# Optimization experiments

Measured on AMD Instinct MI355X. Metric: run time of the kernel, lower is better.

## Reference

```python
import jax, jax.numpy as jnp
import numpy as np

B, T, EMB, HS = 512, 256, 364, 64

def setup_inputs() -> dict:
    key = jax.random.key(0)
    ks = jax.random.split(key, 7)
    s = EMB ** -0.5  # keep weight scale sane
    return {
        "x": jax.random.normal(ks[0], (B, T, EMB), jnp.float32),
        "Wk": jax.random.normal(ks[1], (EMB, HS), jnp.float32) * s,
        "bk": jax.random.normal(ks[2], (HS,), jnp.float32) * 0.01,
        "Wq": jax.random.normal(ks[3], (EMB, HS), jnp.float32) * s,
        "bq": jax.random.normal(ks[4], (HS,), jnp.float32) * 0.01,
        "Wv": jax.random.normal(ks[5], (EMB, HS), jnp.float32) * s,
        "bv": jax.random.normal(ks[6], (HS,), jnp.float32) * 0.01,
    }

def reference(x, Wk, bk, Wq, bq, Wv, bv):
    # Faithful to the original: wei = k @ q^T (note swapped q/k vs textbook),
    # scaled by head_size**-0.5, causal mask, softmax, (dropout = identity in eval), then @ v.
    k = x @ Wk + bk          # [B, T, HS]
    q = x @ Wq + bq          # [B, T, HS]
    v = x @ Wv + bv          # [B, T, HS]
    scale = k.shape[-1] ** -0.5
    wei = jnp.einsum('btd,bsd->bts', k, q) * scale  # [B, T, T]
    causal = jnp.tril(jnp.ones((T, T), dtype=bool))
    wei = jnp.where(causal, wei, -jnp.inf)
    wei = jax.nn.softmax(wei, axis=-1)
    out = jnp.einsum('bts,bsd->btd', wei, v)        # [B, T, HS]
    return out
```

## Files before the change

### kernel.cpp

```cpp
#include <hip/hip_runtime.h>
#include <math.h>

#define BB   512
#define TT   256
#define EMBD 364
#define HS   64
#define KPAD 384
#define NC   192

typedef __attribute__((ext_vector_type(8))) short short8_t;
typedef __attribute__((ext_vector_type(4))) float f32x4;

__device__ __forceinline__ ushort f2bf(float v) {
    union { float f; unsigned u; } c; c.f = v;
    unsigned b = c.u;
    return (ushort)((b + 0x7FFF + ((b >> 16) & 1)) >> 16);
}
__device__ __forceinline__ ushort f2bfc(float v) {
    union { float f; unsigned u; } c; c.f = v;
    return (ushort)((c.u + 0x8000u) >> 16);
}

#define GLOAD_LDS16(GP, LP)                                                       \
    __builtin_amdgcn_global_load_lds(                                             \
        (const __attribute__((address_space(1))) void*)(const void*)(GP),         \
        (__attribute__((address_space(3))) void*)(void*)(LP), 16, 0, 0)

#define WTR_BYTES ((size_t)144 * 512 * 2)
#define KQ_ELEMS  ((size_t)BB * TT * HS)
#define K_OFF_B   (WTR_BYTES)
#define Q_OFF_B   (K_OFF_B + KQ_ELEMS * 2)
#define VT_OFF_B  (Q_OFF_B + KQ_ELEMS * 2)

__global__ void prep_wtr(const float* __restrict__ Wk, const float* __restrict__ Wq,
                         const float* __restrict__ Wv, ushort* __restrict__ WTr)
{
    const int bid = blockIdx.x;
    const int jj  = bid / 12;
    const int t   = bid % 12;
    const int l   = threadIdx.x;
    const int c   = jj * 16 + (l & 15);
    const float* Wp = (c < 64) ? Wk : (c < 128 ? Wq : Wv);
    const float s   = (c < 64) ? 0.125f : 1.0f;
    const int col   = c & 63;
    #pragma unroll
    for (int i = 0; i < 8; ++i) {
        int k = t * 32 + (l >> 4) * 8 + i;
        float v = (k < EMBD) ? Wp[(size_t)k * HS + col] * s : 0.f;
        WTr[((size_t)bid * 64 + l) * 8 + i] = f2bf(v);
    }
}

__global__ __launch_bounds__(256, 3) void proj_gemm(
    const float* __restrict__ x, const ushort* __restrict__ WTr,
    const float* __restrict__ bk_, const float* __restrict__ bq_,
    const float* __restrict__ bv_,
    ushort* __restrict__ Kg, ushort* __restrict__ Qg, ushort* __restrict__ Vt)
{
    const int blk = blockIdx.x;
    const int tid = threadIdx.x;
    const int l   = tid & 63;
    const int w   = tid >> 6;
    const int l15 = l & 15;
    const int lg  = l >> 4;

    __shared__ float xf[32 * KPAD];

    const float* xb = x + (size_t)blk * 32 * EMBD;

    #pragma unroll
    for (int gi = 0; gi < 12; ++gi) {
        const int g     = w * 12 + gi;
        const unsigned flatP = (unsigned)(g * 64 + l);
        const unsigned row   = flatP / 96u;
        const unsigned p     = flatP % 96u;
        const unsigned q     = p ^ (row & 7u);
        const unsigned colq  = (q < 91u) ? q : 0u;
        const float* gp = xb + (size_t)row * EMBD + colq * 4u;
        GLOAD_LDS16(gp, (char*)xf + (size_t)g * 1024);
    }

    float bias3[3];
    #pragma unroll
    for (int j = 0; j < 3; ++j) {
        int c = w * 48 + j * 16 + l15;
        bias3[j] = (c < 64) ? bk_[c] * 0.125f : (c < 128 ? bq_[c - 64] : bv_[c - 128]);
    }

    f32x4 acc[2][3];
    #pragma unroll
    for (int mi = 0; mi < 2; ++mi)
        #pragma unroll
        for (int j = 0; j < 3; ++j) acc[mi][j] = (f32x4){0.f, 0.f, 0.f, 0.f};

    __syncthreads();

    #pragma unroll
    for (int ks = 0; ks < 12; ++ks) {
        short8_t Bf[3];
        #pragma unroll
        for (int j = 0; j < 3; ++j)
            Bf[j] = *(const short8_t*)&WTr[(((size_t)(w * 3 + j) * 12 + ks) * 64 + l) * 8];
        #pragma unroll
        for (int mi = 0; mi < 2; ++mi) {
            const unsigned row = mi * 16 + l15;
            const unsigned q0  = ks * 8 + lg * 2;
            const unsigned p0  = q0 ^ (row & 7u);
            const unsigned p1  = (q0 + 1u) ^ (row & 7u);
            f32x4 A0 = *(const f32x4*)&xf[row * KPAD + p0 * 4u];
            f32x4 A1 = *(const f32x4*)&xf[row * KPAD + p1 * 4u];
            union { short8_t s8; ushort us[8]; } pk;
            pk.us[0] = f2bfc(A0[0]); pk.us[1] = f2bfc(A0[1]);
            pk.us[2] = f2bfc(A0[2]); pk.us[3] = f2bfc(A0[3]);
            pk.us[4] = f2bfc(A1[0]); pk.us[5] = f2bfc(A1[1]);
            pk.us[6] = f2bfc(A1[2]); pk.us[7] = f2bfc(A1[3]);
            #pragma unroll
            for (int j = 0; j < 3; ++j)
                acc[mi][j] = __builtin_amdgcn_mfma_f32_16x16x32_bf16(pk.s8, Bf[j], acc[mi][j], 0, 0, 0);
        }
    }

    const int b   = blk >> 3;
    const int tl0 = (blk & 7) * 32;
    #pragma unroll
    for (int j = 0; j < 3; ++j) {
        const int c = w * 48 + j * 16 + l15;
        #pragma unroll
        for (int mi = 0; mi < 2; ++mi) {
            if (c < 64) {
                #pragma unroll
                for (int r = 0; r < 4; ++r) {
                    const size_t trow = (size_t)blk * 32 + mi * 16 + lg * 4 + r;
                    Kg[trow * HS + c] = f2bf(acc[mi][j][r] + bias3[j]);
                }
            } else if (c < 128) {
                #pragma unroll
                for (int r = 0; r < 4; ++r) {
                    const size_t trow = (size_t)blk * 32 + mi * 16 + lg * 4 + r;
                    Qg[trow * HS + (c - 64)] = f2bf(acc[mi][j][r] + bias3[j]);
                }
            } else {
                ushort4 pk;
                pk.x = f2bf(acc[mi][j][0] + bias3[j]);
                pk.y = f2bf(acc[mi][j][1] + bias3[j]);
                pk.z = f2bf(acc[mi][j][2] + bias3[j]);
                pk.w = f2bf(acc[mi][j][3] + bias3[j]);
                *(ushort4*)&Vt[((size_t)b * HS + (c - 128)) * TT + tl0 + mi * 16 + lg * 4] = pk;
            }
        }
    }
}

__global__ __launch_bounds__(512, 4) void attn_fused(
    const ushort* __restrict__ Kg, const ushort* __restrict__ Qg,
    const ushort* __restrict__ Vt, float* __restrict__ out)
{
    const int b   = blockIdx.x;
    const int tid = threadIdx.x;
    const int l   = tid & 63;
    const int w   = tid >> 6;
    const int l15 = l & 15;
    const int lg  = l >> 4;

    __shared__ ushort pb[8][16 * 40];
    ushort* pbw = pb[w];

    const ushort* Kb = Kg + (size_t)b * TT * HS;
    const ushort* Qb = Qg + (size_t)b * TT * HS;
    const ushort* Vb = Vt + (size_t)b * HS * TT;

    #pragma unroll
    for (int half = 0; half < 2; ++half) {
        const int rt = half ? (15 - w) : w;
        const int t0 = rt * 16;

        short8_t afr[2];
        afr[0] = *(const short8_t*)&Kb[(t0 + l15) * HS + lg * 8];
        afr[1] = *(const short8_t*)&Kb[(t0 + l15) * HS + 32 + lg * 8];

        float mr[4], lr[4];
        f32x4 o[4];
        #pragma unroll
        for (int r = 0; r < 4; ++r) { mr[r] = -INFINITY; lr[r] = 0.f; }
        #pragma unroll
        for (int nt = 0; nt < 4; ++nt) o[nt] = (f32x4){0.f, 0.f, 0.f, 0.f};

        const int jd = t0 >> 5;
        for (int j = 0; j <= jd; ++j) {
            const int sb = j * 32;
            f32x4 sacc[2];
            sacc[0] = (f32x4){0.f, 0.f, 0.f, 0.f};
            sacc[1] = (f32x4){0.f, 0.f, 0.f, 0.f};
            #pragma unroll
            for (int kk = 0; kk < 2; ++kk) {
                #pragma unroll
                for (int ct = 0; ct < 2; ++ct) {
                    short8_t bfr = *(const short8_t*)&Qb[(sb + ct * 16 + l15) * HS + kk * 32 + lg * 8];
                    sacc[ct] = __builtin_amdgcn_mfma_f32_16x16x32_bf16(afr[kk], bfr, sacc[ct], 0, 0, 0);
                }
            }
            #pragma unroll
            for (int ct = 0; ct < 2; ++ct) {
                int s = sb + ct * 16 + l15;
                #pragma unroll
                for (int r = 0; r < 4; ++r) {
                    int t = t0 + lg * 4 + r;
                    if (s > t) sacc[ct][r] = -INFINITY;
                }
            }
            float p0[4], p1[4], fsc[4];
            #pragma unroll
            for (int r = 0; r < 4; ++r) {
                float mx = fmaxf(sacc[0][r], sacc[1][r]);
                mx = fmaxf(mx, __shfl_xor(mx, 1));
                mx = fmaxf(mx, __shfl_xor(mx, 2));
                mx = fmaxf(mx, __shfl_xor(mx, 4));
                mx = fmaxf(mx, __shfl_xor(mx, 8));
                float nm = fmaxf(mr[r], mx);
                fsc[r] = __expf(mr[r] - nm);
                mr[r] = nm;
                p0[r] = __expf(sacc[0][r] - nm);
                p1[r] = __expf(sacc[1][r] - nm);
                float ps = p0[r] + p1[r];
                ps += __shfl_xor(ps, 1);
                ps += __shfl_xor(ps, 2);
                ps += __shfl_xor(ps, 4);
                ps += __shfl_xor(ps, 8);
                lr[r] = lr[r] * fsc[r] + ps;
            }
            #pragma unroll
            for (int nt = 0; nt < 4; ++nt)
                #pragma unroll
                for (int r = 0; r < 4; ++r) o[nt][r] *= fsc[r];
            #pragma unroll
            for (int r = 0; r < 4; ++r) {
                pbw[(lg * 4 + r) * 40 + l15]      = f2bf(p0[r]);
                pbw[(lg * 4 + r) * 40 + 16 + l15] = f2bf(p1[r]);
            }
            short8_t pa = *(const short8_t*)&pbw[l15 * 40 + lg * 8];
            #pragma unroll
            for (int nt = 0; nt < 4; ++nt) {
                short8_t bfr = *(const short8_t*)&Vb[(nt * 16 + l15) * TT + sb + lg * 8];
                o[nt] = __builtin_amdgcn_mfma_f32_16x16x32_bf16(pa, bfr, o[nt], 0, 0, 0);
            }
        }
        #pragma unroll
        for (int r = 0; r < 4; ++r) {
            float inv = 1.0f / lr[r];
            int t = t0 + lg * 4 + r;
            float* op = out + ((size_t)b * TT + t) * HS;
            #pragma unroll
            for (int nt = 0; nt < 4; ++nt)
                op[nt * 16 + l15] = o[nt][r] * inv;
        }
    }
}

extern "C" void kernel_launch(void* const* d_in, const int* in_sizes, int n_in,
                              void* d_out, int out_size, void* d_ws, size_t ws_size,
                              hipStream_t stream) {
    const float* x  = (const float*)d_in[0];
    const float* Wk = (const float*)d_in[1];
    const float* bk = (const float*)d_in[2];
    const float* Wq = (const float*)d_in[3];
    const float* bq = (const float*)d_in[4];
    const float* Wv = (const float*)d_in[5];
    const float* bv = (const float*)d_in[6];
    float* out = (float*)d_out;

    ushort* WTr = (ushort*)d_ws;
    ushort* Kg  = (ushort*)((char*)d_ws + K_OFF_B);
    ushort* Qg  = (ushort*)((char*)d_ws + Q_OFF_B);
    ushort* Vt  = (ushort*)((char*)d_ws + VT_OFF_B);

    prep_wtr<<<dim3(144), dim3(64), 0, stream>>>(Wk, Wq, Wv, WTr);
    proj_gemm<<<dim3(4096), dim3(256), 0, stream>>>(x, WTr, bk, bq, bv, Kg, Qg, Vt);
    attn_fused<<<dim3(BB), dim3(512), 0, stream>>>(Kg, Qg, Vt, out);
}
```

Before: 112.2 us.

## Split projection into separate bf16 cast pass and bf16-input GEMM

Adds an xcast kernel that converts x to padded bf16 in workspace, then a proj_bf GEMM that loads bf16 rows into LDS and feeds MFMA directly, removing the per-tile fp32-to-bf16 conversion and halving LDS footprint so more blocks fit per CU. It costs an extra full pass over x (read fp32 plus write and re-read bf16, about 100MB of extra traffic) and an extra launch. The old fp32 path remains as a fallback when the workspace is too small.

```diff
diff --git a/kernel.cpp b/kernel.cpp
--- a/kernel.cpp
+++ b/kernel.cpp
@@ -16,10 +16,6 @@
     unsigned b = c.u;
     return (ushort)((b + 0x7FFF + ((b >> 16) & 1)) >> 16);
 }
-__device__ __forceinline__ ushort f2bfc(float v) {
-    union { float f; unsigned u; } c; c.f = v;
-    return (ushort)((c.u + 0x8000u) >> 16);
-}
 
 #define GLOAD_LDS16(GP, LP)                                                       \
     __builtin_amdgcn_global_load_lds(                                             \
@@ -31,6 +27,9 @@
 #define K_OFF_B   (WTR_BYTES)
 #define Q_OFF_B   (K_OFF_B + KQ_ELEMS * 2)
 #define VT_OFF_B  (Q_OFF_B + KQ_ELEMS * 2)
+#define XB_OFF_B  (VT_OFF_B + KQ_ELEMS * 2)
+#define XB_BYTES  ((size_t)BB * TT * KPAD * 2)
+#define WS_NEED2  (XB_OFF_B + XB_BYTES)
 
 __global__ void prep_wtr(const float* __restrict__ Wk, const float* __restrict__ Wq,
                          const float* __restrict__ Wv, ushort* __restrict__ WTr)
@@ -51,8 +50,28 @@
     }
 }
 
-__global__ __launch_bounds__(256, 3) void proj_gemm(
-    const float* __restrict__ x, const ushort* __restrict__ WTr,
+__global__ __launch_bounds__(256, 8) void xcast(
+    const float* __restrict__ x, ushort* __restrict__ Xb)
+{
+    const size_t r0 = (size_t)blockIdx.x * 32;
+    #pragma unroll
+    for (int it = 0; it < 12; ++it) {
+        int f = it * 256 + threadIdx.x;
+        int row = f / 96;
+        int p   = f - row * 96;
+        ushort4 o;
+        if (p < 91) {
+            float4 v = *(const float4*)&x[(r0 + row) * EMBD + p * 4];
+            o.x = f2bf(v.x); o.y = f2bf(v.y); o.z = f2bf(v.z); o.w = f2bf(v.w);
+        } else {
+            o.x = 0; o.y = 0; o.z = 0; o.w = 0;
+        }
+        *(ushort4*)&Xb[(r0 + row) * KPAD + p * 4] = o;
+    }
+}
+
+__global__ __launch_bounds__(256, 4) void proj_bf(
+    const ushort* __restrict__ Xb, const ushort* __restrict__ WTr,
     const float* __restrict__ bk_, const float* __restrict__ bq_,
     const float* __restrict__ bv_,
     ushort* __restrict__ Kg, ushort* __restrict__ Qg, ushort* __restrict__ Vt)
@@ -64,10 +83,98 @@
     const int l15 = l & 15;
     const int lg  = l >> 4;
 
+    __shared__ ushort xt[32 * 392];
+
+    const ushort* xb = Xb + (size_t)blk * 32 * KPAD;
+
+    for (int g = w; g < 25; g += 4) {
+        int f   = g * 64 + l;
+        if (f < 1568) {
+            int row = f / 49;
+            int p   = f - row * 49;
+            int col = (p < 48) ? p * 8 : 0;
+            GLOAD_LDS16(xb + (size_t)row * KPAD + col, (char*)xt + (size_t)g * 1024);
+        }
+    }
+
+    float bias3[3];
+    #pragma unroll
+    for (int j = 0; j < 3; ++j) {
+        int c = w * 48 + j * 16 + l15;
+        bias3[j] = (c < 64) ? bk_[c] * 0.125f : (c < 128 ? bq_[c - 64] : bv_[c - 128]);
+    }
+
+    f32x4 acc[2][3];
+    #pragma unroll
+    for (int mi = 0; mi < 2; ++mi)
+        #pragma unroll
+        for (int j = 0; j < 3; ++j) acc[mi][j] = (f32x4){0.f, 0.f, 0.f, 0.f};
+
+    __syncthreads();
+
+    #pragma unroll
+    for (int ks = 0; ks < 12; ++ks) {
+        short8_t Bf[3];
+        #pragma unroll
+        for (int j = 0; j < 3; ++j)
+            Bf[j] = *(const short8_t*)&WTr[(((size_t)(w * 3 + j) * 12 + ks) * 64 + l) * 8];
+        #pragma unroll
+        for (int mi = 0; mi < 2; ++mi) {
+            const int row = mi * 16 + l15;
+            short8_t a = *(const short8_t*)((const char*)xt + row * 784 + (ks * 4 + lg) * 16);
+            #pragma unroll
+            for (int j = 0; j < 3; ++j)
+                acc[mi][j] = __builtin_amdgcn_mfma_f32_16x16x32_bf16(a, Bf[j], acc[mi][j], 0, 0, 0);
+        }
+    }
+
+    const int b   = blk >> 3;
+    const int tl0 = (blk & 7) * 32;
+    #pragma unroll
+    for (int j = 0; j < 3; ++j) {
+        const int c = w * 48 + j * 16 + l15;
+        #pragma unroll
+        for (int mi = 0; mi < 2; ++mi) {
+            if (c < 64) {
+                #pragma unroll
+                for (int r = 0; r < 4; ++r) {
+                    const size_t trow = (size_t)blk * 32 + mi * 16 + lg * 4 + r;
+                    Kg[trow * HS + c] = f2bf(acc[mi][j][r] + bias3[j]);
+                }
+            } else if (c < 128) {
+                #pragma unroll
+                for (int r = 0; r < 4; ++r) {
+                    const size_t trow = (size_t)blk * 32 + mi * 16 + lg * 4 + r;
+                    Qg[trow * HS + (c - 64)] = f2bf(acc[mi][j][r] + bias3[j]);
+                }
+            } else {
+                ushort4 pk;
+                pk.x = f2bf(acc[mi][j][0] + bias3[j]);
+                pk.y = f2bf(acc[mi][j][1] + bias3[j]);
+                pk.z = f2bf(acc[mi][j][2] + bias3[j]);
+                pk.w = f2bf(acc[mi][j][3] + bias3[j]);
+                *(ushort4*)&Vt[((size_t)b * HS + (c - 128)) * TT + tl0 + mi * 16 + lg * 4] = pk;
+            }
+        }
+    }
+}
+
+__global__ __launch_bounds__(256, 3) void proj_f32(
+    const float* __restrict__ x, const ushort* __restrict__ WTr,
+    const float* __restrict__ bk_, const float* __restrict__ bq_,
+    const float* __restrict__ bv_,
+    ushort* __restrict__ Kg, ushort* __restrict__ Qg, ushort* __restrict__ Vt)
+{
+    const int blk = blockIdx.x;
+    const int tid = threadIdx.x;
+    const int l   = tid & 63;
+    const int w   = tid >> 6;
+    const int l15 = l & 15;
+    const int lg  = l >> 4;
+
     __shared__ float xf[32 * KPAD];
 
     const float* xb = x + (size_t)blk * 32 * EMBD;
-
     #pragma unroll
     for (int gi = 0; gi < 12; ++gi) {
         const int g     = w * 12 + gi;
@@ -76,8 +183,7 @@
         const unsigned p     = flatP % 96u;
         const unsigned q     = p ^ (row & 7u);
         const unsigned colq  = (q < 91u) ? q : 0u;
-        const float* gp = xb + (size_t)row * EMBD + colq * 4u;
-        GLOAD_LDS16(gp, (char*)xf + (size_t)g * 1024);
+        GLOAD_LDS16(xb + (size_t)row * EMBD + colq * 4u, (char*)xf + (size_t)g * 1024);
     }
 
     float bias3[3];
@@ -86,13 +192,11 @@
         int c = w * 48 + j * 16 + l15;
         bias3[j] = (c < 64) ? bk_[c] * 0.125f : (c < 128 ? bq_[c - 64] : bv_[c - 128]);
     }
-
     f32x4 acc[2][3];
     #pragma unroll
     for (int mi = 0; mi < 2; ++mi)
         #pragma unroll
         for (int j = 0; j < 3; ++j) acc[mi][j] = (f32x4){0.f, 0.f, 0.f, 0.f};
-
     __syncthreads();
 
     #pragma unroll
@@ -110,10 +214,15 @@
             f32x4 A0 = *(const f32x4*)&xf[row * KPAD + p0 * 4u];
             f32x4 A1 = *(const f32x4*)&xf[row * KPAD + p1 * 4u];
             union { short8_t s8; ushort us[8]; } pk;
-            pk.us[0] = f2bfc(A0[0]); pk.us[1] = f2bfc(A0[1]);
-            pk.us[2] = f2bfc(A0[2]); pk.us[3] = f2bfc(A0[3]);
-            pk.us[4] = f2bfc(A1[0]); pk.us[5] = f2bfc(A1[1]);
-            pk.us[6] = f2bfc(A1[2]); pk.us[7] = f2bfc(A1[3]);
+            union { float f; unsigned u; } cv;
+            cv.f = A0[0]; pk.us[0] = (ushort)((cv.u + 0x8000u) >> 16);
+            cv.f = A0[1]; pk.us[1] = (ushort)((cv.u + 0x8000u) >> 16);
+            cv.f = A0[2]; pk.us[2] = (ushort)((cv.u + 0x8000u) >> 16);
+            cv.f = A0[3]; pk.us[3] = (ushort)((cv.u + 0x8000u) >> 16);
+            cv.f = A1[0]; pk.us[4] = (ushort)((cv.u + 0x8000u) >> 16);
+            cv.f = A1[1]; pk.us[5] = (ushort)((cv.u + 0x8000u) >> 16);
+            cv.f = A1[2]; pk.us[6] = (ushort)((cv.u + 0x8000u) >> 16);
+            cv.f = A1[3]; pk.us[7] = (ushort)((cv.u + 0x8000u) >> 16);
             #pragma unroll
             for (int j = 0; j < 3; ++j)
                 acc[mi][j] = __builtin_amdgcn_mfma_f32_16x16x32_bf16(pk.s8, Bf[j], acc[mi][j], 0, 0, 0);
@@ -274,6 +383,13 @@
     ushort* Vt  = (ushort*)((char*)d_ws + VT_OFF_B);
 
     prep_wtr<<<dim3(144), dim3(64), 0, stream>>>(Wk, Wq, Wv, WTr);
-    proj_gemm<<<dim3(4096), dim3(256), 0, stream>>>(x, WTr, bk, bq, bv, Kg, Qg, Vt);
+
+    if (ws_size >= WS_NEED2) {
+        ushort* Xb = (ushort*)((char*)d_ws + XB_OFF_B);
+        xcast<<<dim3(4096), dim3(256), 0, stream>>>(x, Xb);
+        proj_bf<<<dim3(4096), dim3(256), 0, stream>>>(Xb, WTr, bk, bq, bv, Kg, Qg, Vt);
+    } else {
+        proj_f32<<<dim3(4096), dim3(256), 0, stream>>>(x, WTr, bk, bq, bv, Kg, Qg, Vt);
+    }
     attn_fused<<<dim3(BB), dim3(512), 0, stream>>>(Kg, Qg, Vt, out);
 }
```

After: 139.6 us. 1.24x slower.
